# Performance work log

Measured on AMD Instinct MI355X. Metric: run time of the kernel, lower is better.

The kernel has to match this reference:

```python
import jax, jax.numpy as jnp
import numpy as np

N_NODES = 50000
N_EDGES = 800000
D_IN = 128
DIM = 128
N_LAYERS = 3
N_GRAPHS = 128


def setup_inputs() -> dict:
    key = jax.random.key(0)
    ks = jax.random.split(key, 10)
    x = jax.random.normal(ks[0], (N_NODES, D_IN), dtype=jnp.float32)
    edge_index = jax.random.randint(ks[1], (2, N_EDGES), 0, N_NODES, dtype=jnp.int64)
    batch = jnp.sort(jax.random.randint(ks[2], (N_NODES,), 0, N_GRAPHS, dtype=jnp.int64))
    def glorot(k, fan_in, fan_out):
        s = jnp.sqrt(6.0 / (fan_in + fan_out))
        return jax.random.uniform(k, (fan_in, fan_out), jnp.float32, -s, s)
    W0 = glorot(ks[3], D_IN, DIM)
    W1 = glorot(ks[4], DIM, DIM)
    W2 = glorot(ks[5], DIM, DIM)
    b0 = jnp.zeros((DIM,), jnp.float32)
    b1 = jnp.zeros((DIM,), jnp.float32)
    b2 = jnp.zeros((DIM,), jnp.float32)
    return {"x": x, "edge_index": edge_index, "batch": batch,
            "W0": W0, "b0": b0, "W1": W1, "b1": b1, "W2": W2, "b2": b2}


def _gcn_norm(edge_index, n_nodes):
    # add self-loops, then symmetric normalization (PyG gcn_norm)
    loops = jnp.arange(n_nodes, dtype=edge_index.dtype)
    src = jnp.concatenate([edge_index[0], loops])
    dst = jnp.concatenate([edge_index[1], loops])
    deg = jax.ops.segment_sum(jnp.ones_like(dst, dtype=jnp.float32), dst,
                              num_segments=n_nodes)
    dinv = jnp.where(deg > 0, jax.lax.rsqrt(deg), 0.0)
    norm = dinv[src] * dinv[dst]  # [E + N]
    return src, dst, norm


def _gcn_conv(x, W, b, src, dst, norm, n_nodes):
    h = x @ W                      # [N, dim]
    msgs = h[src] * norm[:, None]  # [E+N, dim] gather + edge scale
    out = jax.ops.segment_sum(msgs, dst, num_segments=n_nodes)  # scatter-add
    return out + b


def reference(x, edge_index, batch, W0, b0, W1, b1, W2, b2):
    n = x.shape[0]
    src, dst, norm = _gcn_norm(edge_index, n)
    Ws, bs = (W0, W1, W2), (b0, b1, b2)
    xs = []
    h = x
    for i in range(N_LAYERS):
        h = jax.nn.relu(_gcn_conv(h, Ws[i], bs[i], src, dst, norm, n))
        xs.append(h)
    # global mean pool per layer output
    counts = jax.ops.segment_sum(jnp.ones((n,), jnp.float32), batch,
                                 num_segments=N_GRAPHS)
    counts = jnp.maximum(counts, 1.0)[:, None]
    xpool = [jax.ops.segment_sum(h, batch, num_segments=N_GRAPHS) / counts
             for h in xs]
    return jnp.concatenate(xpool, axis=1), jnp.concatenate(xs, axis=1)
```

## Files before the change

### kernel.cpp

```cpp
#include <hip/hip_runtime.h>

#define NNODES 50000
#define NEDGES 800000
#define DIM 128
#define NGRAPHS 128
#define OUT1_STRIDE 384
#define OUT0_ELEMS (NGRAPHS * OUT1_STRIDE)
#define SCAN_CHUNK 512
#define ROWPAD 50048

typedef unsigned int uint;
typedef unsigned short ushort;
typedef short bf16x8 __attribute__((ext_vector_type(8)));
typedef float f32x4 __attribute__((ext_vector_type(4)));

union U4 { uint4 u; bf16x8 h; };

__device__ inline uint rne_bf16(float f) {
    uint b = __float_as_uint(f);
    return (b + 0x7fffu + ((b >> 16) & 1u)) >> 16;
}
__device__ inline uint pack_bf16(float lo, float hi) {
    return rne_bf16(lo) | (rne_bf16(hi) << 16);
}
__device__ inline float blo(uint u) { return __uint_as_float(u << 16); }
__device__ inline float bhi(uint u) { return __uint_as_float(u & 0xffff0000u); }

__global__ __launch_bounds__(256) void k_pre(const float* __restrict__ W0,
                                             const float* __restrict__ W1,
                                             const float* __restrict__ W2,
                                             uint* __restrict__ wz,
                                             int* __restrict__ rowcnt,
                                             uint* __restrict__ hb, int N) {
    if (blockIdx.x >= 24) {
        int i = (blockIdx.x - 24) * 256 + threadIdx.x;
        if (i < N) rowcnt[i] = 0;
        if (i < 64) hb[(size_t)N * 64 + i] = 0;
        return;
    }
    int layer = blockIdx.x >> 3;
    const float* W = (layer == 0) ? W0 : ((layer == 1) ? W1 : W2);
    int t = (blockIdx.x & 7) * 256 + threadIdx.x;
    int f = t >> 6, lane = t & 63;
    int kb = f >> 3, nt = f & 7;
    int q = lane >> 4, m = lane & 15;
    int col = nt * 16 + m;
    uint v[8];
#pragma unroll
    for (int j = 0; j < 8; ++j)
        v[j] = rne_bf16(W[(kb * 32 + q * 8 + j) * 128 + col]);
    uint4 o;
    o.x = v[0] | (v[1] << 16);
    o.y = v[2] | (v[3] << 16);
    o.z = v[4] | (v[5] << 16);
    o.w = v[6] | (v[7] << 16);
    ((uint4*)wz)[layer * 2048 + t] = o;
}

__global__ void k_count(const int* __restrict__ dst, int* __restrict__ rowcnt,
                        int* __restrict__ rank, int E) {
    int e = blockIdx.x * blockDim.x + threadIdx.x;
    if (e < E) rank[e] = atomicAdd(&rowcnt[dst[e]], 1);
}

__global__ __launch_bounds__(512) void k_sum(const int* __restrict__ cnt,
                                             int* __restrict__ bsum,
                                             float* __restrict__ dinv, int n) {
    __shared__ int red[512];
    int t = threadIdx.x;
    int i = blockIdx.x * SCAN_CHUNK + t;
    int c = (i < n) ? cnt[i] : 0;
    if (i < n) dinv[i] = rsqrtf((float)c + 1.0f);
    red[t] = c;
    __syncthreads();
    for (int off = 256; off > 0; off >>= 1) {
        if (t < off) red[t] += red[t + off];
        __syncthreads();
    }
    if (t == 0) bsum[blockIdx.x] = red[0];
}

__global__ __launch_bounds__(128) void k_scanb(const int* __restrict__ bsum,
                                               int* __restrict__ boff, int nb) {
    __shared__ int s[128];
    int t = threadIdx.x;
    int v = (t < nb) ? bsum[t] : 0;
    s[t] = v;
    __syncthreads();
    for (int off = 1; off < 128; off <<= 1) {
        int u = (t >= off) ? s[t - off] : 0;
        __syncthreads();
        s[t] += u;
        __syncthreads();
    }
    boff[t] = s[t] - v;
    if (t == nb - 1) boff[nb] = s[t];
}

__global__ __launch_bounds__(512) void k_writeptr(const int* __restrict__ cnt,
                                                  const int* __restrict__ boff,
                                                  int* __restrict__ rowptr, int n) {
    __shared__ int s[512];
    int t = threadIdx.x;
    int i = blockIdx.x * SCAN_CHUNK + t;
    int v = (i < n) ? cnt[i] : 0;
    s[t] = v;
    __syncthreads();
    for (int off = 1; off < 512; off <<= 1) {
        int u = (t >= off) ? s[t - off] : 0;
        __syncthreads();
        s[t] += u;
        __syncthreads();
    }
    if (i < n) rowptr[i] = boff[blockIdx.x] + s[t] - v;
    if (i == n - 1) rowptr[n] = boff[blockIdx.x] + s[t];
}

__global__ void k_fill(const int* __restrict__ src, const int* __restrict__ dst,
                       const int* __restrict__ rowptr, const int* __restrict__ rank,
                       int* __restrict__ csr_src, int E) {
    int e = blockIdx.x * blockDim.x + threadIdx.x;
    if (e < E) {
        int d = dst[e];
        csr_src[rowptr[d] + rank[e]] = src[e];
    }
}

__global__ __launch_bounds__(256) void k_gemm(const float* __restrict__ A, int lda,
                                              const uint* __restrict__ Wswz,
                                              const float* __restrict__ dinv,
                                              uint* __restrict__ hb, int M) {
    __shared__ uint4 wsw[2048];
    __shared__ ushort cbuf[64 * 128];
    int tid = threadIdx.x;
#pragma unroll
    for (int i = 0; i < 8; ++i)
        wsw[i * 256 + tid] = ((const uint4*)Wswz)[i * 256 + tid];
    __syncthreads();
    int wave = tid >> 6, lane = tid & 63;
    int q = lane >> 4, m = lane & 15;
    int row0 = blockIdx.x * 64 + wave * 16;
    int arow = min(row0 + m, M - 1);
    const float* Ar = A + (size_t)arow * lda + q * 8;
    f32x4 zero = {0.0f, 0.0f, 0.0f, 0.0f};
    f32x4 acc[8];
#pragma unroll
    for (int i = 0; i < 8; ++i) acc[i] = zero;
#pragma unroll
    for (int kb = 0; kb < 4; ++kb) {
        float4 f0 = *(const float4*)(Ar + kb * 32);
        float4 f1 = *(const float4*)(Ar + kb * 32 + 4);
        U4 a;
        a.u.x = pack_bf16(f0.x, f0.y);
        a.u.y = pack_bf16(f0.z, f0.w);
        a.u.z = pack_bf16(f1.x, f1.y);
        a.u.w = pack_bf16(f1.z, f1.w);
#pragma unroll
        for (int nt = 0; nt < 8; ++nt) {
            U4 b; b.u = wsw[(kb * 8 + nt) * 64 + lane];
            acc[nt] = __builtin_amdgcn_mfma_f32_16x16x32_bf16(a.h, b.h, acc[nt], 0, 0, 0);
        }
    }
    float dv[4];
#pragma unroll
    for (int r = 0; r < 4; ++r)
        dv[r] = dinv[min(row0 + q * 4 + r, M - 1)];
    ushort* cw = cbuf + wave * 16 * 128;
#pragma unroll
    for (int nt = 0; nt < 8; ++nt)
#pragma unroll
        for (int r = 0; r < 4; ++r)
            cw[(q * 4 + r) * 128 + nt * 16 + m] = (ushort)rne_bf16(acc[nt][r] * dv[r]);
    __syncthreads();
    const uint4* cr4 = (const uint4*)cbuf;
#pragma unroll
    for (int i = 0; i < 4; ++i) {
        int c = (wave * 256) + i * 64 + lane;
        int grow = blockIdx.x * 64 + (c >> 4);
        uint4 v = cr4[c];
        if (grow < M) ((uint4*)hb)[(size_t)grow * 16 + (c & 15)] = v;
    }
}

__global__ __launch_bounds__(256) void k_agg(const uint* __restrict__ hb,
                                             const int* __restrict__ rowptr,
                                             const int* __restrict__ csr_src,
                                             const float* __restrict__ dinv,
                                             const float* __restrict__ bias,
                                             float* __restrict__ out1,
                                             int N, int layer) {
    int wave = threadIdx.x >> 6;
    int lane = threadIdx.x & 63;
    int n = blockIdx.x * 4 + wave;
    if (n >= N) return;
    int g16 = lane >> 4;
    int m16 = lane & 15;
    const uint4* hb4 = (const uint4*)hb;

    uint4 su = hb4[(size_t)n * 16 + m16];
    float sel = (g16 == 0) ? 1.0f : 0.0f;
    float a0 = sel * blo(su.x), a1 = sel * bhi(su.x);
    float a2 = sel * blo(su.y), a3 = sel * bhi(su.y);
    float a4 = sel * blo(su.z), a5 = sel * bhi(su.z);
    float a6 = sel * blo(su.w), a7 = sel * bhi(su.w);

    int beg = rowptr[n], end = rowptr[n + 1];
    for (int base = beg; base < end; base += 16) {
        int s0, s1, s2, s3;
        {
            int e0 = base + 0 + g16;
            int e1 = base + 4 + g16;
            int e2 = base + 8 + g16;
            int e3 = base + 12 + g16;
            s0 = (e0 < end) ? csr_src[e0] : N;
            s1 = (e1 < end) ? csr_src[min(e1, end - 1)] : N;
            s2 = (e2 < end) ? csr_src[min(e2, end - 1)] : N;
            s3 = (e3 < end) ? csr_src[min(e3, end - 1)] : N;
        }
        uint4 u0 = hb4[(size_t)s0 * 16 + m16];
        uint4 u1 = hb4[(size_t)s1 * 16 + m16];
        uint4 u2 = hb4[(size_t)s2 * 16 + m16];
        uint4 u3 = hb4[(size_t)s3 * 16 + m16];
        a0 += blo(u0.x); a1 += bhi(u0.x); a2 += blo(u0.y); a3 += bhi(u0.y);
        a4 += blo(u0.z); a5 += bhi(u0.z); a6 += blo(u0.w); a7 += bhi(u0.w);
        a0 += blo(u1.x); a1 += bhi(u1.x); a2 += blo(u1.y); a3 += bhi(u1.y);
        a4 += blo(u1.z); a5 += bhi(u1.z); a6 += blo(u1.w); a7 += bhi(u1.w);
        a0 += blo(u2.x); a1 += bhi(u2.x); a2 += blo(u2.y); a3 += bhi(u2.y);
        a4 += blo(u2.z); a5 += bhi(u2.z); a6 += blo(u2.w); a7 += bhi(u2.w);
        a0 += blo(u3.x); a1 += bhi(u3.x); a2 += blo(u3.y); a3 += bhi(u3.y);
        a4 += blo(u3.z); a5 += bhi(u3.z); a6 += blo(u3.w); a7 += bhi(u3.w);
    }

#pragma unroll
    for (int d = 16; d < 64; d <<= 1) {
        a0 += __shfl_xor(a0, d); a1 += __shfl_xor(a1, d);
        a2 += __shfl_xor(a2, d); a3 += __shfl_xor(a3, d);
        a4 += __shfl_xor(a4, d); a5 += __shfl_xor(a5, d);
        a6 += __shfl_xor(a6, d); a7 += __shfl_xor(a7, d);
    }

    float vx = (g16 == 0) ? a0 : (g16 == 1) ? a2 : (g16 == 2) ? a4 : a6;
    float vy = (g16 == 0) ? a1 : (g16 == 1) ? a3 : (g16 == 2) ? a5 : a7;
    float din = dinv[n];
    float2 b = ((const float2*)bias)[m16 * 4 + g16];
    float ox = fmaxf(din * vx + b.x, 0.0f);
    float oy = fmaxf(din * vy + b.y, 0.0f);
    size_t o1 = (size_t)n * OUT1_STRIDE + layer * DIM + (m16 * 8 + g16 * 2);
    *(float2*)(out1 + o1) = make_float2(ox, oy);
}

__global__ __launch_bounds__(256) void k_pool(const float* __restrict__ out1,
                                              const int* __restrict__ batch,
                                              float* __restrict__ out0, int N) {
    int g = blockIdx.x / 3;
    int chunk = blockIdx.x % 3;
    int lo = 0, hi = N;
    while (lo < hi) { int mid = (lo + hi) >> 1; if (batch[mid] < g) lo = mid + 1; else hi = mid; }
    int beg = lo;
    hi = N;
    while (lo < hi) { int mid = (lo + hi) >> 1; if (batch[mid] < g + 1) lo = mid + 1; else hi = mid; }
    int end = lo;
    int t = threadIdx.x;
    int ch = t & 127;
    int slice = t >> 7;
    const float* p = out1 + (size_t)chunk * 128 + ch;
    float acc = 0.0f;
    int i = beg + slice;
    for (; i + 6 < end; i += 8) {
        float a0 = p[(size_t)i * OUT1_STRIDE];
        float a1 = p[(size_t)(i + 2) * OUT1_STRIDE];
        float a2 = p[(size_t)(i + 4) * OUT1_STRIDE];
        float a3 = p[(size_t)(i + 6) * OUT1_STRIDE];
        acc += (a0 + a1) + (a2 + a3);
    }
    for (; i < end; i += 2) acc += p[(size_t)i * OUT1_STRIDE];
    __shared__ float red[256];
    red[t] = acc;
    __syncthreads();
    if (t < 128) {
        float tot = red[t] + red[t + 128];
        float cnt = (float)(end - beg);
        out0[(size_t)g * OUT1_STRIDE + chunk * 128 + t] = tot / fmaxf(cnt, 1.0f);
    }
}

extern "C" void kernel_launch(void* const* d_in, const int* in_sizes, int n_in,
                              void* d_out, int out_size, void* d_ws, size_t ws_size,
                              hipStream_t stream) {
    const float* x     = (const float*)d_in[0];
    const int*   ei    = (const int*)d_in[1];
    const int*   batch = (const int*)d_in[2];
    const float* W0 = (const float*)d_in[3];
    const float* b0 = (const float*)d_in[4];
    const float* W1 = (const float*)d_in[5];
    const float* b1 = (const float*)d_in[6];
    const float* W2 = (const float*)d_in[7];
    const float* b2 = (const float*)d_in[8];
    (void)n_in; (void)ws_size; (void)out_size;

    const int E = in_sizes[1] / 2;
    const int N = in_sizes[2];
    const int* src = ei;
    const int* dst = ei + E;

    char* ws = (char*)d_ws;
    uint*  hb       = (uint*)ws;  ws += (size_t)ROWPAD * 64 * 4;
    uint*  wz       = (uint*)ws;  ws += 3 * 8192 * 4;
    float* dinv     = (float*)ws; ws += 50016 * 4;
    int*   rowcnt   = (int*)ws;   ws += 50016 * 4;
    int*   rowptr   = (int*)ws;   ws += 50016 * 4;
    int*   rank     = (int*)ws;   ws += (size_t)NEDGES * 4;
    int*   csr_src  = (int*)ws;   ws += (size_t)NEDGES * 4;
    int*   bsum     = (int*)ws;   ws += 256 * 4;
    int*   boff     = (int*)ws;   ws += 256 * 4;

    float* out0 = (float*)d_out;
    float* out1 = (float*)d_out + OUT0_ELEMS;

    const int nb  = (N + SCAN_CHUNK - 1) / SCAN_CHUNK;
    const int nbz = 24 + (N + 255) / 256;

    k_pre     <<<nbz, 256, 0, stream>>>(W0, W1, W2, wz, rowcnt, hb, N);
    k_count   <<<(E + 255) / 256, 256, 0, stream>>>(dst, rowcnt, rank, E);
    k_sum     <<<nb, 512, 0, stream>>>(rowcnt, bsum, dinv, N);
    k_scanb   <<<1, 128, 0, stream>>>(bsum, boff, nb);
    k_writeptr<<<nb, 512, 0, stream>>>(rowcnt, boff, rowptr, N);
    k_fill    <<<(E + 255) / 256, 256, 0, stream>>>(src, dst, rowptr, rank, csr_src, E);

    const float* bs[3] = {b0, b1, b2};
    const int ngb = (N + 63) / 64;
    for (int l = 0; l < 3; ++l) {
        const float* Ain = (l == 0) ? x : (out1 + (size_t)(l - 1) * DIM);
        int lda          = (l == 0) ? DIM : OUT1_STRIDE;
        k_gemm<<<ngb, 256, 0, stream>>>(Ain, lda, wz + l * 8192, dinv, hb, N);
        k_agg <<<(N + 3) / 4, 256, 0, stream>>>(hb, rowptr, csr_src, dinv,
                                                bs[l], out1, N, l);
    }
    k_pool<<<NGRAPHS * 3, 256, 0, stream>>>(out1, batch, out0, N);
}
```

Before: 310.1 us.

## Split bf16 feature table into four column slices for sliced aggregation

The GEMM now writes the bf16 hidden features in a column-sliced layout: four slices of 32 features, each a contiguous ROWPAD-row table, including the zero sentinel row. The aggregation kernel launches a 2D grid with one slice per blockIdx.y, so each wave gathers 64-byte slice rows for 16 edges at a time instead of 256-byte full rows for 4 edges. This shrinks each gathered working set so it fits L2/MALL better and gives more memory-level parallelism per wave. In exchange, rowptr and csr_src are read four times, the wave reduction needs more shuffle steps, and four times as many blocks are launched.

```diff
diff --git a/kernel.cpp b/kernel.cpp
--- a/kernel.cpp
+++ b/kernel.cpp
@@ -25,6 +25,7 @@
 }
 __device__ inline float blo(uint u) { return __uint_as_float(u << 16); }
 __device__ inline float bhi(uint u) { return __uint_as_float(u & 0xffff0000u); }
+
 
 __global__ __launch_bounds__(256) void k_pre(const float* __restrict__ W0,
                                              const float* __restrict__ W1,
@@ -35,7 +36,8 @@
     if (blockIdx.x >= 24) {
         int i = (blockIdx.x - 24) * 256 + threadIdx.x;
         if (i < N) rowcnt[i] = 0;
-        if (i < 64) hb[(size_t)N * 64 + i] = 0;
+        if (i < 64)
+            hb[(size_t)(i >> 4) * (ROWPAD * 16) + (size_t)N * 16 + (i & 15)] = 0;
         return;
     }
     int layer = blockIdx.x >> 3;
@@ -173,12 +175,15 @@
             cw[(q * 4 + r) * 128 + nt * 16 + m] = (ushort)rne_bf16(acc[nt][r] * dv[r]);
     __syncthreads();
     const uint4* cr4 = (const uint4*)cbuf;
+    uint4* hb4 = (uint4*)hb;
 #pragma unroll
     for (int i = 0; i < 4; ++i) {
         int c = (wave * 256) + i * 64 + lane;
         int grow = blockIdx.x * 64 + (c >> 4);
+        int p = c & 15;
         uint4 v = cr4[c];
-        if (grow < M) ((uint4*)hb)[(size_t)grow * 16 + (c & 15)] = v;
+        if (grow < M)
+            hb4[(size_t)(p >> 2) * (ROWPAD * 4) + (size_t)grow * 4 + (p & 3)] = v;
     }
 }
 
@@ -191,62 +196,66 @@
                                              int N, int layer) {
     int wave = threadIdx.x >> 6;
     int lane = threadIdx.x & 63;
+    int slice = blockIdx.y;
     int n = blockIdx.x * 4 + wave;
     if (n >= N) return;
-    int g16 = lane >> 4;
-    int m16 = lane & 15;
-    const uint4* hb4 = (const uint4*)hb;
-
-    uint4 su = hb4[(size_t)n * 16 + m16];
-    float sel = (g16 == 0) ? 1.0f : 0.0f;
+    int g = lane >> 2;
+    int q4 = lane & 3;
+    const uint4* hb4 = (const uint4*)hb + (size_t)slice * (ROWPAD * 4);
+
+    uint4 su = hb4[(size_t)n * 4 + q4];
+    float sel = (g == 0) ? 1.0f : 0.0f;
     float a0 = sel * blo(su.x), a1 = sel * bhi(su.x);
     float a2 = sel * blo(su.y), a3 = sel * bhi(su.y);
     float a4 = sel * blo(su.z), a5 = sel * bhi(su.z);
     float a6 = sel * blo(su.w), a7 = sel * bhi(su.w);
 
     int beg = rowptr[n], end = rowptr[n + 1];
-    for (int base = beg; base < end; base += 16) {
-        int s0, s1, s2, s3;
-        {
-            int e0 = base + 0 + g16;
-            int e1 = base + 4 + g16;
-            int e2 = base + 8 + g16;
-            int e3 = base + 12 + g16;
-            s0 = (e0 < end) ? csr_src[e0] : N;
-            s1 = (e1 < end) ? csr_src[min(e1, end - 1)] : N;
-            s2 = (e2 < end) ? csr_src[min(e2, end - 1)] : N;
-            s3 = (e3 < end) ? csr_src[min(e3, end - 1)] : N;
-        }
-        uint4 u0 = hb4[(size_t)s0 * 16 + m16];
-        uint4 u1 = hb4[(size_t)s1 * 16 + m16];
-        uint4 u2 = hb4[(size_t)s2 * 16 + m16];
-        uint4 u3 = hb4[(size_t)s3 * 16 + m16];
+    int base = beg;
+    for (; base + 32 <= end; base += 32) {
+        int s0 = csr_src[base + g];
+        int s1 = csr_src[base + 16 + g];
+        uint4 u0 = hb4[(size_t)s0 * 4 + q4];
+        uint4 u1 = hb4[(size_t)s1 * 4 + q4];
         a0 += blo(u0.x); a1 += bhi(u0.x); a2 += blo(u0.y); a3 += bhi(u0.y);
         a4 += blo(u0.z); a5 += bhi(u0.z); a6 += blo(u0.w); a7 += bhi(u0.w);
         a0 += blo(u1.x); a1 += bhi(u1.x); a2 += blo(u1.y); a3 += bhi(u1.y);
         a4 += blo(u1.z); a5 += bhi(u1.z); a6 += blo(u1.w); a7 += bhi(u1.w);
-        a0 += blo(u2.x); a1 += bhi(u2.x); a2 += blo(u2.y); a3 += bhi(u2.y);
-        a4 += blo(u2.z); a5 += bhi(u2.z); a6 += blo(u2.w); a7 += bhi(u2.w);
-        a0 += blo(u3.x); a1 += bhi(u3.x); a2 += blo(u3.y); a3 += bhi(u3.y);
-        a4 += blo(u3.z); a5 += bhi(u3.z); a6 += blo(u3.w); a7 += bhi(u3.w);
-    }
-
-#pragma unroll
-    for (int d = 16; d < 64; d <<= 1) {
+    }
+    for (; base < end; base += 16) {
+        int e = base + g;
+        int s0 = (e < end) ? csr_src[e] : N;
+        uint4 u0 = hb4[(size_t)s0 * 4 + q4];
+        a0 += blo(u0.x); a1 += bhi(u0.x); a2 += blo(u0.y); a3 += bhi(u0.y);
+        a4 += blo(u0.z); a5 += bhi(u0.z); a6 += blo(u0.w); a7 += bhi(u0.w);
+    }
+
+#pragma unroll
+    for (int d = 4; d < 64; d <<= 1) {
         a0 += __shfl_xor(a0, d); a1 += __shfl_xor(a1, d);
         a2 += __shfl_xor(a2, d); a3 += __shfl_xor(a3, d);
         a4 += __shfl_xor(a4, d); a5 += __shfl_xor(a5, d);
         a6 += __shfl_xor(a6, d); a7 += __shfl_xor(a7, d);
     }
 
-    float vx = (g16 == 0) ? a0 : (g16 == 1) ? a2 : (g16 == 2) ? a4 : a6;
-    float vy = (g16 == 0) ? a1 : (g16 == 1) ? a3 : (g16 == 2) ? a5 : a7;
-    float din = dinv[n];
-    float2 b = ((const float2*)bias)[m16 * 4 + g16];
-    float ox = fmaxf(din * vx + b.x, 0.0f);
-    float oy = fmaxf(din * vy + b.y, 0.0f);
-    size_t o1 = (size_t)n * OUT1_STRIDE + layer * DIM + (m16 * 8 + g16 * 2);
-    *(float2*)(out1 + o1) = make_float2(ox, oy);
+    if (g == 0) {
+        float din = dinv[n];
+        int c0 = slice * 32 + q4 * 8;
+        float4 b0 = *(const float4*)(bias + c0);
+        float4 b1 = *(const float4*)(bias + c0 + 4);
+        float4 o0, o1;
+        o0.x = fmaxf(din * a0 + b0.x, 0.0f);
+        o0.y = fmaxf(din * a1 + b0.y, 0.0f);
+        o0.z = fmaxf(din * a2 + b0.z, 0.0f);
+        o0.w = fmaxf(din * a3 + b0.w, 0.0f);
+        o1.x = fmaxf(din * a4 + b1.x, 0.0f);
+        o1.y = fmaxf(din * a5 + b1.y, 0.0f);
+        o1.z = fmaxf(din * a6 + b1.z, 0.0f);
+        o1.w = fmaxf(din * a7 + b1.w, 0.0f);
+        float* op = out1 + (size_t)n * OUT1_STRIDE + layer * DIM + c0;
+        *(float4*)op = o0;
+        *(float4*)(op + 4) = o1;
+    }
 }
 
 __global__ __launch_bounds__(256) void k_pool(const float* __restrict__ out1,
@@ -333,8 +342,8 @@
         const float* Ain = (l == 0) ? x : (out1 + (size_t)(l - 1) * DIM);
         int lda          = (l == 0) ? DIM : OUT1_STRIDE;
         k_gemm<<<ngb, 256, 0, stream>>>(Ain, lda, wz + l * 8192, dinv, hb, N);
-        k_agg <<<(N + 3) / 4, 256, 0, stream>>>(hb, rowptr, csr_src, dinv,
-                                                bs[l], out1, N, l);
+        k_agg <<<dim3((N + 3) / 4, 4), 256, 0, stream>>>(hb, rowptr, csr_src, dinv,
+                                                         bs[l], out1, N, l);
     }
     k_pool<<<NGRAPHS * 3, 256, 0, stream>>>(out1, batch, out0, N);
 }
```

Measured after the change: 439.9 us. 41.8% more time.

## Fold block scan into writeptr, use atomic cursors for CSR fill, vectorize index loads

Applied to the files above, without the earlier changes.

Merges the single-block scan kernel into k_writeptr, where each block redundantly scans the block sums, which removes one launch. CSR construction now claims slots with an atomic cursor per row instead of keeping a per-edge rank array, which drops the rank write and read. The aggregation kernel loads neighbor indices as aligned int4 quads with range masks instead of scalar loads, and writes its output with nontemporal stores. Edge order within a row becomes nondeterministic, so float summation order can vary from run to run.

```diff
diff --git a/kernel.cpp b/kernel.cpp
--- a/kernel.cpp
+++ b/kernel.cpp
@@ -13,6 +13,7 @@
 typedef unsigned short ushort;
 typedef short bf16x8 __attribute__((ext_vector_type(8)));
 typedef float f32x4 __attribute__((ext_vector_type(4)));
+typedef float f32x2 __attribute__((ext_vector_type(2)));
 
 union U4 { uint4 u; bf16x8 h; };
 
@@ -57,10 +58,9 @@
     ((uint4*)wz)[layer * 2048 + t] = o;
 }
 
-__global__ void k_count(const int* __restrict__ dst, int* __restrict__ rowcnt,
-                        int* __restrict__ rank, int E) {
+__global__ void k_count(const int* __restrict__ dst, int* __restrict__ rowcnt, int E) {
     int e = blockIdx.x * blockDim.x + threadIdx.x;
-    if (e < E) rank[e] = atomicAdd(&rowcnt[dst[e]], 1);
+    if (e < E) atomicAdd(&rowcnt[dst[e]], 1);
 }
 
 __global__ __launch_bounds__(512) void k_sum(const int* __restrict__ cnt,
@@ -80,28 +80,23 @@
     if (t == 0) bsum[blockIdx.x] = red[0];
 }
 
-__global__ __launch_bounds__(128) void k_scanb(const int* __restrict__ bsum,
-                                               int* __restrict__ boff, int nb) {
-    __shared__ int s[128];
+__global__ __launch_bounds__(512) void k_writeptr(const int* __restrict__ cnt,
+                                                  const int* __restrict__ bsum,
+                                                  int* __restrict__ rowptr,
+                                                  int* __restrict__ rowcur,
+                                                  int n, int nb) {
+    __shared__ int s[512];
+    __shared__ int sb[128];
     int t = threadIdx.x;
-    int v = (t < nb) ? bsum[t] : 0;
-    s[t] = v;
+    if (t < 128) sb[t] = (t < nb) ? bsum[t] : 0;
     __syncthreads();
     for (int off = 1; off < 128; off <<= 1) {
-        int u = (t >= off) ? s[t - off] : 0;
-        __syncthreads();
-        s[t] += u;
-        __syncthreads();
-    }
-    boff[t] = s[t] - v;
-    if (t == nb - 1) boff[nb] = s[t];
-}
-
-__global__ __launch_bounds__(512) void k_writeptr(const int* __restrict__ cnt,
-                                                  const int* __restrict__ boff,
-                                                  int* __restrict__ rowptr, int n) {
-    __shared__ int s[512];
-    int t = threadIdx.x;
+        int u = (t < 128 && t >= off) ? sb[t - off] : 0;
+        __syncthreads();
+        if (t < 128) sb[t] += u;
+        __syncthreads();
+    }
+    int boffb = (blockIdx.x == 0) ? 0 : sb[blockIdx.x - 1];
     int i = blockIdx.x * SCAN_CHUNK + t;
     int v = (i < n) ? cnt[i] : 0;
     s[t] = v;
@@ -112,17 +107,20 @@
         s[t] += u;
         __syncthreads();
     }
-    if (i < n) rowptr[i] = boff[blockIdx.x] + s[t] - v;
-    if (i == n - 1) rowptr[n] = boff[blockIdx.x] + s[t];
+    if (i < n) {
+        int p = boffb + s[t] - v;
+        rowptr[i] = p;
+        rowcur[i] = p;
+    }
+    if (i == n - 1) rowptr[n] = boffb + s[t];
 }
 
 __global__ void k_fill(const int* __restrict__ src, const int* __restrict__ dst,
-                       const int* __restrict__ rowptr, const int* __restrict__ rank,
-                       int* __restrict__ csr_src, int E) {
+                       int* __restrict__ rowcur, int* __restrict__ csr_src, int E) {
     int e = blockIdx.x * blockDim.x + threadIdx.x;
     if (e < E) {
-        int d = dst[e];
-        csr_src[rowptr[d] + rank[e]] = src[e];
+        int pos = atomicAdd(&rowcur[dst[e]], 1);
+        csr_src[pos] = src[e];
     }
 }
 
@@ -197,56 +195,65 @@
     int m16 = lane & 15;
     const uint4* hb4 = (const uint4*)hb;
 
+    int beg = rowptr[n], end = rowptr[n + 1];
     uint4 su = hb4[(size_t)n * 16 + m16];
+
+    float2 a0, a1, a2, a3;
     float sel = (g16 == 0) ? 1.0f : 0.0f;
-    float a0 = sel * blo(su.x), a1 = sel * bhi(su.x);
-    float a2 = sel * blo(su.y), a3 = sel * bhi(su.y);
-    float a4 = sel * blo(su.z), a5 = sel * bhi(su.z);
-    float a6 = sel * blo(su.w), a7 = sel * bhi(su.w);
-
-    int beg = rowptr[n], end = rowptr[n + 1];
-    for (int base = beg; base < end; base += 16) {
-        int s0, s1, s2, s3;
-        {
-            int e0 = base + 0 + g16;
-            int e1 = base + 4 + g16;
-            int e2 = base + 8 + g16;
-            int e3 = base + 12 + g16;
-            s0 = (e0 < end) ? csr_src[e0] : N;
-            s1 = (e1 < end) ? csr_src[min(e1, end - 1)] : N;
-            s2 = (e2 < end) ? csr_src[min(e2, end - 1)] : N;
-            s3 = (e3 < end) ? csr_src[min(e3, end - 1)] : N;
-        }
+    a0 = make_float2(sel * blo(su.x), sel * bhi(su.x));
+    a1 = make_float2(sel * blo(su.y), sel * bhi(su.y));
+    a2 = make_float2(sel * blo(su.z), sel * bhi(su.z));
+    a3 = make_float2(sel * blo(su.w), sel * bhi(su.w));
+
+    const int4* csr4 = (const int4*)csr_src;
+    int q0 = beg >> 2;
+    int qn = (end + 3) >> 2;
+    for (int q = q0; q < qn; q += 4) {
+        int qe = q + g16;
+        int4 sv = csr4[qe];
+        int e0 = qe * 4;
+        int s0 = (e0     >= beg && e0     < end) ? sv.x : N;
+        int s1 = (e0 + 1 >= beg && e0 + 1 < end) ? sv.y : N;
+        int s2 = (e0 + 2 >= beg && e0 + 2 < end) ? sv.z : N;
+        int s3 = (e0 + 3 >= beg && e0 + 3 < end) ? sv.w : N;
         uint4 u0 = hb4[(size_t)s0 * 16 + m16];
         uint4 u1 = hb4[(size_t)s1 * 16 + m16];
         uint4 u2 = hb4[(size_t)s2 * 16 + m16];
         uint4 u3 = hb4[(size_t)s3 * 16 + m16];
-        a0 += blo(u0.x); a1 += bhi(u0.x); a2 += blo(u0.y); a3 += bhi(u0.y);
-        a4 += blo(u0.z); a5 += bhi(u0.z); a6 += blo(u0.w); a7 += bhi(u0.w);
-        a0 += blo(u1.x); a1 += bhi(u1.x); a2 += blo(u1.y); a3 += bhi(u1.y);
-        a4 += blo(u1.z); a5 += bhi(u1.z); a6 += blo(u1.w); a7 += bhi(u1.w);
-        a0 += blo(u2.x); a1 += bhi(u2.x); a2 += blo(u2.y); a3 += bhi(u2.y);
-        a4 += blo(u2.z); a5 += bhi(u2.z); a6 += blo(u2.w); a7 += bhi(u2.w);
-        a0 += blo(u3.x); a1 += bhi(u3.x); a2 += blo(u3.y); a3 += bhi(u3.y);
-        a4 += blo(u3.z); a5 += bhi(u3.z); a6 += blo(u3.w); a7 += bhi(u3.w);
+        a0.x += blo(u0.x); a0.y += bhi(u0.x);
+        a1.x += blo(u0.y); a1.y += bhi(u0.y);
+        a2.x += blo(u0.z); a2.y += bhi(u0.z);
+        a3.x += blo(u0.w); a3.y += bhi(u0.w);
+        a0.x += blo(u1.x); a0.y += bhi(u1.x);
+        a1.x += blo(u1.y); a1.y += bhi(u1.y);
+        a2.x += blo(u1.z); a2.y += bhi(u1.z);
+        a3.x += blo(u1.w); a3.y += bhi(u1.w);
+        a0.x += blo(u2.x); a0.y += bhi(u2.x);
+        a1.x += blo(u2.y); a1.y += bhi(u2.y);
+        a2.x += blo(u2.z); a2.y += bhi(u2.z);
+        a3.x += blo(u2.w); a3.y += bhi(u2.w);
+        a0.x += blo(u3.x); a0.y += bhi(u3.x);
+        a1.x += blo(u3.y); a1.y += bhi(u3.y);
+        a2.x += blo(u3.z); a2.y += bhi(u3.z);
+        a3.x += blo(u3.w); a3.y += bhi(u3.w);
     }
 
 #pragma unroll
     for (int d = 16; d < 64; d <<= 1) {
-        a0 += __shfl_xor(a0, d); a1 += __shfl_xor(a1, d);
-        a2 += __shfl_xor(a2, d); a3 += __shfl_xor(a3, d);
-        a4 += __shfl_xor(a4, d); a5 += __shfl_xor(a5, d);
-        a6 += __shfl_xor(a6, d); a7 += __shfl_xor(a7, d);
-    }
-
-    float vx = (g16 == 0) ? a0 : (g16 == 1) ? a2 : (g16 == 2) ? a4 : a6;
-    float vy = (g16 == 0) ? a1 : (g16 == 1) ? a3 : (g16 == 2) ? a5 : a7;
+        a0.x += __shfl_xor(a0.x, d); a0.y += __shfl_xor(a0.y, d);
+        a1.x += __shfl_xor(a1.x, d); a1.y += __shfl_xor(a1.y, d);
+        a2.x += __shfl_xor(a2.x, d); a2.y += __shfl_xor(a2.y, d);
+        a3.x += __shfl_xor(a3.x, d); a3.y += __shfl_xor(a3.y, d);
+    }
+
+    float2 pr = (g16 == 0) ? a0 : (g16 == 1) ? a1 : (g16 == 2) ? a2 : a3;
     float din = dinv[n];
     float2 b = ((const float2*)bias)[m16 * 4 + g16];
-    float ox = fmaxf(din * vx + b.x, 0.0f);
-    float oy = fmaxf(din * vy + b.y, 0.0f);
+    f32x2 o;
+    o.x = fmaxf(din * pr.x + b.x, 0.0f);
+    o.y = fmaxf(din * pr.y + b.y, 0.0f);
     size_t o1 = (size_t)n * OUT1_STRIDE + layer * DIM + (m16 * 8 + g16 * 2);
-    *(float2*)(out1 + o1) = make_float2(ox, oy);
+    __builtin_nontemporal_store(o, (f32x2*)(out1 + o1));
 }
 
 __global__ __launch_bounds__(256) void k_pool(const float* __restrict__ out1,
@@ -309,10 +316,9 @@
     float* dinv     = (float*)ws; ws += 50016 * 4;
     int*   rowcnt   = (int*)ws;   ws += 50016 * 4;
     int*   rowptr   = (int*)ws;   ws += 50016 * 4;
-    int*   rank     = (int*)ws;   ws += (size_t)NEDGES * 4;
-    int*   csr_src  = (int*)ws;   ws += (size_t)NEDGES * 4;
+    int*   rowcur   = (int*)ws;   ws += 50016 * 4;
+    int*   csr_src  = (int*)ws;   ws += ((size_t)NEDGES + 64) * 4;
     int*   bsum     = (int*)ws;   ws += 256 * 4;
-    int*   boff     = (int*)ws;   ws += 256 * 4;
 
     float* out0 = (float*)d_out;
     float* out1 = (float*)d_out + OUT0_ELEMS;
@@ -321,11 +327,10 @@
     const int nbz = 24 + (N + 255) / 256;
 
     k_pre     <<<nbz, 256, 0, stream>>>(W0, W1, W2, wz, rowcnt, hb, N);
-    k_count   <<<(E + 255) / 256, 256, 0, stream>>>(dst, rowcnt, rank, E);
+    k_count   <<<(E + 255) / 256, 256, 0, stream>>>(dst, rowcnt, E);
     k_sum     <<<nb, 512, 0, stream>>>(rowcnt, bsum, dinv, N);
-    k_scanb   <<<1, 128, 0, stream>>>(bsum, boff, nb);
-    k_writeptr<<<nb, 512, 0, stream>>>(rowcnt, boff, rowptr, N);
-    k_fill    <<<(E + 255) / 256, 256, 0, stream>>>(src, dst, rowptr, rank, csr_src, E);
+    k_writeptr<<<nb, 512, 0, stream>>>(rowcnt, bsum, rowptr, rowcur, N, nb);
+    k_fill    <<<(E + 255) / 256, 256, 0, stream>>>(src, dst, rowcur, csr_src, E);
 
     const float* bs[3] = {b0, b1, b2};
     const int ngb = (N + 63) / 64;
```

New measurement: 362.9 us. 17.0% more time.
